# Kernel optimization log

Measured on AMD Instinct MI355X. Metric: run time of the kernel, lower is better.

## Reference

```python
import jax, jax.numpy as jnp
import numpy as np

N_NODES = 100000
N_EDGES = 1600000
D = 128
NEG_SLOPE = 0.01  # torch F.leaky_relu default


def setup_inputs() -> dict:
    key = jax.random.key(0)
    k1, k2, k3, k4, k5 = jax.random.split(key, 5)
    nfeat = jax.random.normal(k1, (N_NODES, D), dtype=jnp.float32)
    edge_src = jax.random.randint(k2, (N_EDGES,), 0, N_NODES, dtype=jnp.int32)
    edge_dst = jax.random.randint(k3, (N_EDGES,), 0, N_NODES, dtype=jnp.int32)
    edge_w = jax.random.uniform(k4, (N_EDGES,), dtype=jnp.float32)
    W = jax.random.normal(k5, (D, D), dtype=jnp.float32) * (1.0 / np.sqrt(D))
    return {"nfeat": nfeat, "edge_src": edge_src, "edge_dst": edge_dst,
            "edge_w": edge_w, "W": W}


def reference(nfeat, edge_src, edge_dst, edge_w, W):
    # message: m_e = h[src_e] * w_e  (u_mul_e)
    msg = nfeat[edge_src] * edge_w[:, None]          # [E, D]
    # reduce: h_neighbor[v] = sum_{e: dst(e)=v} m_e  (fn.sum)
    h_neighbor = jax.ops.segment_sum(msg, edge_dst, num_segments=nfeat.shape[0])  # [N, D]
    # Bi-interaction residual: leaky_relu(Linear(h * h_neighbor)); dropout = identity (eval)
    out = jax.nn.leaky_relu((nfeat * h_neighbor) @ W.T, negative_slope=NEG_SLOPE)
    return out
```

## Files before the change

### kernel.cpp

```cpp
#include <hip/hip_runtime.h>
#include <hip/hip_fp16.h>

#define NNODES 100000
#define NEDGES 1600000
#define DIM    128
#define NEG_SLOPE 0.01f
#define NB_SCAN ((NNODES + 1023) / 1024)
#define NPART 8
#define PART_SZ ((NNODES + NPART - 1) / NPART)
#define GEMM_TILES ((NNODES + 63) / 64)

typedef _Float16     v8h __attribute__((ext_vector_type(8)));
typedef float        v4f __attribute__((ext_vector_type(4)));
typedef int          v4i __attribute__((ext_vector_type(4)));
typedef int          v2i __attribute__((ext_vector_type(2)));
typedef float        v4x __attribute__((ext_vector_type(4)));
typedef unsigned int v2u __attribute__((ext_vector_type(2)));
typedef unsigned int v4u __attribute__((ext_vector_type(4)));

static inline size_t align256(size_t x) { return (x + 255) & ~(size_t)255; }

union HU { unsigned int u; __half2 h; };

__global__ __launch_bounds__(256) void zero_f32(float* __restrict__ p, int n4) {
    int i = blockIdx.x * blockDim.x + threadIdx.x;
    int stride = gridDim.x * blockDim.x;
    float4 z = make_float4(0.f, 0.f, 0.f, 0.f);
    for (; i < n4; i += stride) ((float4*)p)[i] = z;
}

__global__ __launch_bounds__(256) void prep(const float* __restrict__ nf,
                                            __half* __restrict__ nf16,
                                            int* __restrict__ counts) {
    int i = blockIdx.x * 256 + threadIdx.x;
    int stride = gridDim.x * 256;
    for (int j = i; j < NNODES * DIM / 4; j += stride) {
        v4x v = __builtin_nontemporal_load((const v4x*)nf + j);
        HU a, b;
        a.h = __float22half2_rn(make_float2(v.x, v.y));
        b.h = __float22half2_rn(make_float2(v.z, v.w));
        ((uint2*)nf16)[j] = make_uint2(a.u, b.u);
    }
    v4i z = (v4i){0, 0, 0, 0};
    for (int j = i; j < NNODES / 4; j += stride)
        *((v4i*)counts + j) = z;
}

__global__ __launch_bounds__(256) void hist_dst4(const int* __restrict__ edst,
                                                 int* __restrict__ counts) {
    int i = blockIdx.x * 256 + threadIdx.x;
    if (i < NEDGES / 4) {
        v4i d = __builtin_nontemporal_load((const v4i*)edst + i);
        atomicAdd(&counts[d.x], 1);
        atomicAdd(&counts[d.y], 1);
        atomicAdd(&counts[d.z], 1);
        atomicAdd(&counts[d.w], 1);
    }
}

__global__ __launch_bounds__(256) void scan1(const int* __restrict__ counts,
                                             int* __restrict__ offsets,
                                             int* __restrict__ blocksum) {
    __shared__ int lds[256];
    int tid = threadIdx.x;
    int base = blockIdx.x * 1024 + tid * 4;
    int c0 = (base + 0 < NNODES) ? counts[base + 0] : 0;
    int c1 = (base + 1 < NNODES) ? counts[base + 1] : 0;
    int c2 = (base + 2 < NNODES) ? counts[base + 2] : 0;
    int c3 = (base + 3 < NNODES) ? counts[base + 3] : 0;
    int t = c0 + c1 + c2 + c3;
    lds[tid] = t;
    __syncthreads();
    for (int d = 1; d < 256; d <<= 1) {
        int v = lds[tid];
        int add = (tid >= d) ? lds[tid - d] : 0;
        __syncthreads();
        lds[tid] = v + add;
        __syncthreads();
    }
    int incl = lds[tid];
    int excl = incl - t;
    if (base + 0 < NNODES) offsets[base + 0] = excl;
    if (base + 1 < NNODES) offsets[base + 1] = excl + c0;
    if (base + 2 < NNODES) offsets[base + 2] = excl + c0 + c1;
    if (base + 3 < NNODES) offsets[base + 3] = excl + c0 + c1 + c2;
    if (tid == 255) blocksum[blockIdx.x] = incl;
}

__global__ __launch_bounds__(128) void scan2p(int* __restrict__ blocksum, int nb) {
    __shared__ int lds[128];
    int tid = threadIdx.x;
    int v = (tid < nb) ? blocksum[tid] : 0;
    lds[tid] = v;
    __syncthreads();
    for (int d = 1; d < 128; d <<= 1) {
        int x = lds[tid];
        int add = (tid >= d) ? lds[tid - d] : 0;
        __syncthreads();
        lds[tid] = x + add;
        __syncthreads();
    }
    if (tid < nb) blocksum[tid] = lds[tid] - v;
}

__global__ __launch_bounds__(256) void scan3(int* __restrict__ offsets,
                                             const int* __restrict__ blocksum,
                                             int* __restrict__ cursor) {
    int add = blocksum[blockIdx.x];
    int base = blockIdx.x * 1024 + threadIdx.x * 4;
    #pragma unroll
    for (int i = 0; i < 4; ++i) {
        int idx = base + i;
        if (idx < NNODES) { int o = offsets[idx] + add; offsets[idx] = o; cursor[idx] = o; }
    }
}

__global__ __launch_bounds__(256) void fill_part(const int* __restrict__ esrc,
                                                 const int* __restrict__ edst,
                                                 const float* __restrict__ ew,
                                                 int* __restrict__ cursor,
                                                 int2* __restrict__ bins) {
    int part = blockIdx.x & (NPART - 1);
    int lo = part * PART_SZ;
    int hi = lo + PART_SZ;
    int t = (blockIdx.x >> 3) * 256 + threadIdx.x;
    int stride = (gridDim.x >> 3) * 256;
    int nq = NEDGES / 4;
    for (int i = t; i < nq; i += stride) {
        v4i d = __builtin_nontemporal_load((const v4i*)edst + i);
        int e = i * 4;
        if (d.x >= lo && d.x < hi) {
            int s = __builtin_nontemporal_load(esrc + e + 0);
            float w = __builtin_nontemporal_load(ew + e + 0);
            int p = atomicAdd(&cursor[d.x], 1);
            bins[p] = make_int2(s, __float_as_int(w));
        }
        if (d.y >= lo && d.y < hi) {
            int s = __builtin_nontemporal_load(esrc + e + 1);
            float w = __builtin_nontemporal_load(ew + e + 1);
            int p = atomicAdd(&cursor[d.y], 1);
            bins[p] = make_int2(s, __float_as_int(w));
        }
        if (d.z >= lo && d.z < hi) {
            int s = __builtin_nontemporal_load(esrc + e + 2);
            float w = __builtin_nontemporal_load(ew + e + 2);
            int p = atomicAdd(&cursor[d.z], 1);
            bins[p] = make_int2(s, __float_as_int(w));
        }
        if (d.w >= lo && d.w < hi) {
            int s = __builtin_nontemporal_load(esrc + e + 3);
            float w = __builtin_nontemporal_load(ew + e + 3);
            int p = atomicAdd(&cursor[d.w], 1);
            bins[p] = make_int2(s, __float_as_int(w));
        }
    }
}

__global__ __launch_bounds__(256) void pull_x16(const __half* __restrict__ nf16,
                                                const int* __restrict__ offsets,
                                                const int* __restrict__ counts,
                                                const int2* __restrict__ bins,
                                                __half* __restrict__ x16) {
    int gid = blockIdx.x * 256 + threadIdx.x;
    int v = gid >> 5;
    int lane = gid & 31;
    if (v >= NNODES) return;
    int start = offsets[v];
    int end = start + counts[v];
    const uint2* nf2 = (const uint2*)nf16;
    float4 a0 = make_float4(0.f, 0.f, 0.f, 0.f);
    float4 a1 = make_float4(0.f, 0.f, 0.f, 0.f);
    float4 a2 = make_float4(0.f, 0.f, 0.f, 0.f);
    float4 a3 = make_float4(0.f, 0.f, 0.f, 0.f);
    int k = start;
    for (; k + 4 <= end; k += 4) {
        v2i e0 = __builtin_nontemporal_load((const v2i*)bins + k);
        v2i e1 = __builtin_nontemporal_load((const v2i*)bins + k + 1);
        v2i e2 = __builtin_nontemporal_load((const v2i*)bins + k + 2);
        v2i e3 = __builtin_nontemporal_load((const v2i*)bins + k + 3);
        uint2 u0 = nf2[(size_t)e0.x * 32 + lane];
        uint2 u1 = nf2[(size_t)e1.x * 32 + lane];
        uint2 u2 = nf2[(size_t)e2.x * 32 + lane];
        uint2 u3 = nf2[(size_t)e3.x * 32 + lane];
        float w0 = __int_as_float(e0.y), w1 = __int_as_float(e1.y);
        float w2 = __int_as_float(e2.y), w3 = __int_as_float(e3.y);
        HU h; float2 f;
        h.u = u0.x; f = __half22float2(h.h); a0.x += w0 * f.x; a0.y += w0 * f.y;
        h.u = u0.y; f = __half22float2(h.h); a0.z += w0 * f.x; a0.w += w0 * f.y;
        h.u = u1.x; f = __half22float2(h.h); a1.x += w1 * f.x; a1.y += w1 * f.y;
        h.u = u1.y; f = __half22float2(h.h); a1.z += w1 * f.x; a1.w += w1 * f.y;
        h.u = u2.x; f = __half22float2(h.h); a2.x += w2 * f.x; a2.y += w2 * f.y;
        h.u = u2.y; f = __half22float2(h.h); a2.z += w2 * f.x; a2.w += w2 * f.y;
        h.u = u3.x; f = __half22float2(h.h); a3.x += w3 * f.x; a3.y += w3 * f.y;
        h.u = u3.y; f = __half22float2(h.h); a3.z += w3 * f.x; a3.w += w3 * f.y;
    }
    for (; k < end; ++k) {
        v2i e = __builtin_nontemporal_load((const v2i*)bins + k);
        float w = __int_as_float(e.y);
        uint2 u = nf2[(size_t)e.x * 32 + lane];
        HU h; float2 f;
        h.u = u.x; f = __half22float2(h.h); a0.x += w * f.x; a0.y += w * f.y;
        h.u = u.y; f = __half22float2(h.h); a0.z += w * f.x; a0.w += w * f.y;
    }
    float4 acc;
    acc.x = (a0.x + a1.x) + (a2.x + a3.x);
    acc.y = (a0.y + a1.y) + (a2.y + a3.y);
    acc.z = (a0.z + a1.z) + (a2.z + a3.z);
    acc.w = (a0.w + a1.w) + (a2.w + a3.w);
    uint2 un = nf2[(size_t)v * 32 + lane];
    HU h; float2 f;
    h.u = un.x; f = __half22float2(h.h); acc.x *= f.x; acc.y *= f.y;
    h.u = un.y; f = __half22float2(h.h); acc.z *= f.x; acc.w *= f.y;
    HU o0, o1;
    o0.h = __float22half2_rn(make_float2(acc.x, acc.y));
    o1.h = __float22half2_rn(make_float2(acc.z, acc.w));
    v2u ov = (v2u){o0.u, o1.u};
    __builtin_nontemporal_store(ov, (v2u*)x16 + (size_t)v * 32 + lane);
}

__global__ __launch_bounds__(256) void gemm16(const __half* __restrict__ x16,
                                              const float* __restrict__ W,
                                              float* __restrict__ out) {
    __shared__ _Float16 Wl[128 * 128];
    __shared__ _Float16 Xl[64 * 128];
    int tid = threadIdx.x;

    const float4* Wg = (const float4*)W;
    for (int i = tid; i < 2048; i += 256) {
        int r = i >> 4, c = i & 15;
        float4 lo = Wg[(r * 128 + c * 8) >> 2];
        float4 hi = Wg[((r * 128 + c * 8) >> 2) + 1];
        v8h h;
        h[0] = (_Float16)lo.x; h[1] = (_Float16)lo.y; h[2] = (_Float16)lo.z; h[3] = (_Float16)lo.w;
        h[4] = (_Float16)hi.x; h[5] = (_Float16)hi.y; h[6] = (_Float16)hi.z; h[7] = (_Float16)hi.w;
        *(v8h*)&Wl[r * 128 + (c ^ (r & 7)) * 8] = h;
    }

    int rbase = blockIdx.x * 64;
    for (int i = tid; i < 1024; i += 256) {
        int r = i >> 4, c = i & 15;
        int grow = rbase + r;
        v4u u = (v4u){0u, 0u, 0u, 0u};
        if (grow < NNODES)
            u = __builtin_nontemporal_load((const v4u*)x16 + (size_t)grow * 16 + c);
        *(v4u*)&Xl[r * 128 + (c ^ (r & 7)) * 8] = u;
    }
    __syncthreads();

    int wave = tid >> 6;
    int lane = tid & 63;
    int n = lane & 15;
    int g = lane >> 4;

    v4f acc[8];
    #pragma unroll
    for (int jb = 0; jb < 8; ++jb) acc[jb] = (v4f){0.f, 0.f, 0.f, 0.f};

    #pragma unroll
    for (int kb = 0; kb < 4; ++kb) {
        v8h a = *(v8h*)&Xl[(wave * 16 + n) * 128 + (((kb * 4 + g) ^ (n & 7)) * 8)];
        #pragma unroll
        for (int jb = 0; jb < 8; ++jb) {
            v8h b = *(v8h*)&Wl[(jb * 16 + n) * 128 + (((kb * 4 + g) ^ (n & 7)) * 8)];
            acc[jb] = __builtin_amdgcn_mfma_f32_16x16x32_f16(a, b, acc[jb], 0, 0, 0);
        }
    }

    int row0 = rbase + wave * 16 + g * 4;
    #pragma unroll
    for (int jb = 0; jb < 8; ++jb) {
        #pragma unroll
        for (int reg = 0; reg < 4; ++reg) {
            int r = row0 + reg;
            if (r < NNODES) {
                float v = acc[jb][reg];
                v = v >= 0.f ? v : NEG_SLOPE * v;
                __builtin_nontemporal_store(v, out + (size_t)r * 128 + jb * 16 + n);
            }
        }
    }
}

__global__ __launch_bounds__(256) void scatter_edges(
    const float* __restrict__ nfeat, const int* __restrict__ esrc,
    const int* __restrict__ edst, const float* __restrict__ ew,
    float* __restrict__ hn) {
    long long t = (long long)blockIdx.x * 256 + threadIdx.x;
    int e = (int)(t >> 5);
    if (e >= NEDGES) return;
    int lane = (int)(t & 31);
    int s = esrc[e];
    int d = edst[e];
    float w = ew[e];
    float4 v = ((const float4*)(nfeat + (size_t)s * DIM))[lane];
    float* o = hn + (size_t)d * DIM + lane * 4;
    unsafeAtomicAdd(o + 0, v.x * w);
    unsafeAtomicAdd(o + 1, v.y * w);
    unsafeAtomicAdd(o + 2, v.z * w);
    unsafeAtomicAdd(o + 3, v.w * w);
}

__global__ __launch_bounds__(256) void elem_mul(const float* __restrict__ nfeat,
                                                float* __restrict__ hn, int n4) {
    int i = blockIdx.x * blockDim.x + threadIdx.x;
    int stride = gridDim.x * blockDim.x;
    for (; i < n4; i += stride) {
        float4 a = ((const float4*)nfeat)[i];
        float4 b = ((float4*)hn)[i];
        b.x *= a.x; b.y *= a.y; b.z *= a.z; b.w *= a.w;
        ((float4*)hn)[i] = b;
    }
}

__global__ __launch_bounds__(256) void bi_gemm2(
    const float* __restrict__ x, const float* __restrict__ W,
    float* __restrict__ out) {
    extern __shared__ float lds[];
    float4* W4  = (float4*)lds;
    float*  xs  = lds + 128 * 128;
    float4* xs4 = (float4*)xs;
    int tid = threadIdx.x;
    const float4* Wg = (const float4*)W;
    for (int i = tid; i < 128 * 32; i += 256) {
        int j = i >> 5, d4 = i & 31;
        W4[(j << 5) | (d4 ^ ((j >> 2) & 7))] = Wg[i];
    }
    __syncthreads();
    int tx = tid & 31, ty = tid >> 5;
    int j0 = tx << 2, r0 = ty << 2;
    int ntiles = NNODES / 32;
    for (int tile = blockIdx.x; tile < ntiles; tile += gridDim.x) {
        int rbase = tile * 32;
        for (int i = tid; i < 32 * 32; i += 256)
            xs4[i] = ((const float4*)x)[(size_t)rbase * 32 + i];
        __syncthreads();
        float acc[4][4];
        #pragma unroll
        for (int r = 0; r < 4; ++r)
            #pragma unroll
            for (int j = 0; j < 4; ++j) acc[r][j] = 0.f;
        #pragma unroll 4
        for (int d4 = 0; d4 < 32; ++d4) {
            float4 xv[4], wv[4];
            #pragma unroll
            for (int r = 0; r < 4; ++r) xv[r] = xs4[((r0 + r) << 5) | d4];
            #pragma unroll
            for (int j = 0; j < 4; ++j) {
                int jj = j0 + j;
                wv[j] = W4[(jj << 5) | (d4 ^ ((jj >> 2) & 7))];
            }
            #pragma unroll
            for (int r = 0; r < 4; ++r)
                #pragma unroll
                for (int j = 0; j < 4; ++j) {
                    acc[r][j] += xv[r].x * wv[j].x;
                    acc[r][j] += xv[r].y * wv[j].y;
                    acc[r][j] += xv[r].z * wv[j].z;
                    acc[r][j] += xv[r].w * wv[j].w;
                }
        }
        __syncthreads();
        #pragma unroll
        for (int r = 0; r < 4; ++r) {
            float4 o;
            o.x = acc[r][0] >= 0.f ? acc[r][0] : NEG_SLOPE * acc[r][0];
            o.y = acc[r][1] >= 0.f ? acc[r][1] : NEG_SLOPE * acc[r][1];
            o.z = acc[r][2] >= 0.f ? acc[r][2] : NEG_SLOPE * acc[r][2];
            o.w = acc[r][3] >= 0.f ? acc[r][3] : NEG_SLOPE * acc[r][3];
            size_t row = (size_t)(rbase + r0 + r);
            ((float4*)out)[row * (DIM / 4) + tx] = o;
        }
    }
}

extern "C" void kernel_launch(void* const* d_in, const int* in_sizes, int n_in,
                              void* d_out, int out_size, void* d_ws, size_t ws_size,
                              hipStream_t stream) {
    const float* nfeat = (const float*)d_in[0];
    const int*   esrc  = (const int*)d_in[1];
    const int*   edst  = (const int*)d_in[2];
    const float* ew    = (const float*)d_in[3];
    const float* W     = (const float*)d_in[4];
    float* out = (float*)d_out;

    size_t off = 0;
    size_t nf16_off = off;     off += align256((size_t)NNODES * DIM * 2);
    size_t x16_off = off;      off += align256((size_t)NNODES * DIM * 2);
    size_t cnt_off = off;      off += align256((size_t)NNODES * 4);
    size_t ofs_off = off;      off += align256((size_t)NNODES * 4);
    size_t cur_off = off;      off += align256((size_t)NNODES * 4);
    size_t bsum_off = off;     off += align256((size_t)NB_SCAN * 4);
    size_t bins_off = off;     off += align256((size_t)NEDGES * 8);
    size_t need = off;

    char* ws = (char*)d_ws;

    if (ws_size >= need) {
        __half* nf16 = (__half*)(ws + nf16_off);
        __half* x16  = (__half*)(ws + x16_off);
        int* counts = (int*)(ws + cnt_off);
        int* offsets = (int*)(ws + ofs_off);
        int* cursor = (int*)(ws + cur_off);
        int* blocksum = (int*)(ws + bsum_off);
        int2* bins = (int2*)(ws + bins_off);

        prep<<<2048, 256, 0, stream>>>(nfeat, nf16, counts);
        int e4grid = (NEDGES / 4 + 255) / 256;
        hist_dst4<<<e4grid, 256, 0, stream>>>(edst, counts);
        scan1<<<NB_SCAN, 256, 0, stream>>>(counts, offsets, blocksum);
        scan2p<<<1, 128, 0, stream>>>(blocksum, NB_SCAN);
        scan3<<<NB_SCAN, 256, 0, stream>>>(offsets, blocksum, cursor);
        fill_part<<<2048, 256, 0, stream>>>(esrc, edst, ew, cursor, bins);
        int pgrid = (NNODES * 32 + 255) / 256;
        pull_x16<<<pgrid, 256, 0, stream>>>(nf16, offsets, counts, bins, x16);
        gemm16<<<GEMM_TILES, 256, 0, stream>>>(x16, W, out);
    } else {
        float* hn = (float*)ws;
        hipFuncSetAttribute((const void*)bi_gemm2,
                            hipFuncAttributeMaxDynamicSharedMemorySize, 81920);
        zero_f32<<<2048, 256, 0, stream>>>(hn, NNODES * DIM / 4);
        int sgrid = (NEDGES * 32 + 255) / 256;
        scatter_edges<<<sgrid, 256, 0, stream>>>(nfeat, esrc, edst, ew, hn);
        elem_mul<<<2048, 256, 0, stream>>>(nfeat, hn, NNODES * DIM / 4);
        bi_gemm2<<<512, 256, 81920, stream>>>(hn, W, out);
    }
}
```

Before: 277.2 us.

## Pre-split edges into per-partition buckets before histogram and CSR fill

Adds a split pass that buckets each edge (dst, src, weight) into one of eight destination partitions, using block-local counting and one global atomic per partition. The histogram and CSR fill kernels then read only their own partition's compact list instead of every fill block scanning the full edge array and filtering. The aim is to cut redundant edge reads and improve atomic locality on the counts and cursor arrays. The cost is an extra 16-byte-per-edge staging buffer and one more pass over the edges. A fixed per-partition capacity (PCAP) silently drops edges if a partition overflows, which only holds for roughly uniform destination distributions.

New measurement: 337.5 us. 1.22x slower.

```diff
diff --git a/kernel.cpp b/kernel.cpp
--- a/kernel.cpp
+++ b/kernel.cpp
@@ -8,6 +8,7 @@
 #define NB_SCAN ((NNODES + 1023) / 1024)
 #define NPART 8
 #define PART_SZ ((NNODES + NPART - 1) / NPART)
+#define PCAP 220000
 #define GEMM_TILES ((NNODES + 63) / 64)
 
 typedef _Float16     v8h __attribute__((ext_vector_type(8)));
@@ -31,7 +32,8 @@
 
 __global__ __launch_bounds__(256) void prep(const float* __restrict__ nf,
                                             __half* __restrict__ nf16,
-                                            int* __restrict__ counts) {
+                                            int* __restrict__ counts,
+                                            int* __restrict__ pcur) {
     int i = blockIdx.x * 256 + threadIdx.x;
     int stride = gridDim.x * 256;
     for (int j = i; j < NNODES * DIM / 4; j += stride) {
@@ -44,17 +46,45 @@
     v4i z = (v4i){0, 0, 0, 0};
     for (int j = i; j < NNODES / 4; j += stride)
         *((v4i*)counts + j) = z;
-}
-
-__global__ __launch_bounds__(256) void hist_dst4(const int* __restrict__ edst,
+    if (i < NPART) pcur[i] = 0;
+}
+
+__global__ __launch_bounds__(256) void split_edges(const int* __restrict__ esrc,
+                                                   const int* __restrict__ edst,
+                                                   const float* __restrict__ ew,
+                                                   int* __restrict__ pcur,
+                                                   int4* __restrict__ triples) {
+    __shared__ int bcnt[NPART];
+    __shared__ int gbase[NPART];
+    int tid = threadIdx.x;
+    int e = blockIdx.x * 256 + tid;
+    int dst = __builtin_nontemporal_load(edst + e);
+    int src = __builtin_nontemporal_load(esrc + e);
+    float w = __builtin_nontemporal_load(ew + e);
+    int part = dst / PART_SZ;
+    if (tid < NPART) bcnt[tid] = 0;
+    __syncthreads();
+    int lrank = atomicAdd(&bcnt[part], 1);
+    __syncthreads();
+    if (tid < NPART) gbase[tid] = atomicAdd(&pcur[tid], bcnt[tid]);
+    __syncthreads();
+    int slot = gbase[part] + lrank;
+    if (slot < PCAP)
+        triples[(size_t)part * PCAP + slot] = make_int4(dst, src, __float_as_int(w), 0);
+}
+
+__global__ __launch_bounds__(256) void hist_part(const int4* __restrict__ triples,
+                                                 const int* __restrict__ pcur,
                                                  int* __restrict__ counts) {
-    int i = blockIdx.x * 256 + threadIdx.x;
-    if (i < NEDGES / 4) {
-        v4i d = __builtin_nontemporal_load((const v4i*)edst + i);
-        atomicAdd(&counts[d.x], 1);
-        atomicAdd(&counts[d.y], 1);
-        atomicAdd(&counts[d.z], 1);
-        atomicAdd(&counts[d.w], 1);
+    int part = blockIdx.x & (NPART - 1);
+    int n = pcur[part];
+    if (n > PCAP) n = PCAP;
+    const int4* base = triples + (size_t)part * PCAP;
+    int t = (blockIdx.x >> 3) * 256 + threadIdx.x;
+    int stride = (gridDim.x >> 3) * 256;
+    for (int i = t; i < n; i += stride) {
+        v4i tr = __builtin_nontemporal_load((const v4i*)base + i);
+        atomicAdd(&counts[tr.x], 1);
     }
 }
 
@@ -115,44 +145,20 @@
     }
 }
 
-__global__ __launch_bounds__(256) void fill_part(const int* __restrict__ esrc,
-                                                 const int* __restrict__ edst,
-                                                 const float* __restrict__ ew,
-                                                 int* __restrict__ cursor,
-                                                 int2* __restrict__ bins) {
+__global__ __launch_bounds__(256) void fill_part2(const int4* __restrict__ triples,
+                                                  const int* __restrict__ pcur,
+                                                  int* __restrict__ cursor,
+                                                  int2* __restrict__ bins) {
     int part = blockIdx.x & (NPART - 1);
-    int lo = part * PART_SZ;
-    int hi = lo + PART_SZ;
+    int n = pcur[part];
+    if (n > PCAP) n = PCAP;
+    const int4* base = triples + (size_t)part * PCAP;
     int t = (blockIdx.x >> 3) * 256 + threadIdx.x;
     int stride = (gridDim.x >> 3) * 256;
-    int nq = NEDGES / 4;
-    for (int i = t; i < nq; i += stride) {
-        v4i d = __builtin_nontemporal_load((const v4i*)edst + i);
-        int e = i * 4;
-        if (d.x >= lo && d.x < hi) {
-            int s = __builtin_nontemporal_load(esrc + e + 0);
-            float w = __builtin_nontemporal_load(ew + e + 0);
-            int p = atomicAdd(&cursor[d.x], 1);
-            bins[p] = make_int2(s, __float_as_int(w));
-        }
-        if (d.y >= lo && d.y < hi) {
-            int s = __builtin_nontemporal_load(esrc + e + 1);
-            float w = __builtin_nontemporal_load(ew + e + 1);
-            int p = atomicAdd(&cursor[d.y], 1);
-            bins[p] = make_int2(s, __float_as_int(w));
-        }
-        if (d.z >= lo && d.z < hi) {
-            int s = __builtin_nontemporal_load(esrc + e + 2);
-            float w = __builtin_nontemporal_load(ew + e + 2);
-            int p = atomicAdd(&cursor[d.z], 1);
-            bins[p] = make_int2(s, __float_as_int(w));
-        }
-        if (d.w >= lo && d.w < hi) {
-            int s = __builtin_nontemporal_load(esrc + e + 3);
-            float w = __builtin_nontemporal_load(ew + e + 3);
-            int p = atomicAdd(&cursor[d.w], 1);
-            bins[p] = make_int2(s, __float_as_int(w));
-        }
+    for (int i = t; i < n; i += stride) {
+        v4i tr = __builtin_nontemporal_load((const v4i*)base + i);
+        int p = atomicAdd(&cursor[tr.x], 1);
+        bins[p] = make_int2(tr.y, tr.z);
     }
 }
 
@@ -281,6 +287,51 @@
     }
 }
 
+__global__ __launch_bounds__(256) void hist_dst4(const int* __restrict__ edst,
+                                                 int* __restrict__ counts) {
+    int i = blockIdx.x * 256 + threadIdx.x;
+    if (i < NEDGES / 4) {
+        int4 d = ((const int4*)edst)[i];
+        atomicAdd(&counts[d.x], 1);
+        atomicAdd(&counts[d.y], 1);
+        atomicAdd(&counts[d.z], 1);
+        atomicAdd(&counts[d.w], 1);
+    }
+}
+
+__global__ __launch_bounds__(256) void fill_part(const int* __restrict__ esrc,
+                                                 const int* __restrict__ edst,
+                                                 const float* __restrict__ ew,
+                                                 int* __restrict__ cursor,
+                                                 int2* __restrict__ bins) {
+    int part = blockIdx.x & (NPART - 1);
+    int lo = part * PART_SZ;
+    int hi = lo + PART_SZ;
+    int t = (blockIdx.x >> 3) * 256 + threadIdx.x;
+    int stride = (gridDim.x >> 3) * 256;
+    int nq = NEDGES / 4;
+    for (int i = t; i < nq; i += stride) {
+        int4 d = ((const int4*)edst)[i];
+        int e = i * 4;
+        if (d.x >= lo && d.x < hi) {
+            int p = atomicAdd(&cursor[d.x], 1);
+            bins[p] = make_int2(esrc[e + 0], __float_as_int(ew[e + 0]));
+        }
+        if (d.y >= lo && d.y < hi) {
+            int p = atomicAdd(&cursor[d.y], 1);
+            bins[p] = make_int2(esrc[e + 1], __float_as_int(ew[e + 1]));
+        }
+        if (d.z >= lo && d.z < hi) {
+            int p = atomicAdd(&cursor[d.z], 1);
+            bins[p] = make_int2(esrc[e + 2], __float_as_int(ew[e + 2]));
+        }
+        if (d.w >= lo && d.w < hi) {
+            int p = atomicAdd(&cursor[d.w], 1);
+            bins[p] = make_int2(esrc[e + 3], __float_as_int(ew[e + 3]));
+        }
+    }
+}
+
 __global__ __launch_bounds__(256) void scatter_edges(
     const float* __restrict__ nfeat, const int* __restrict__ esrc,
     const int* __restrict__ edst, const float* __restrict__ ew,
@@ -389,28 +440,42 @@
     size_t cnt_off = off;      off += align256((size_t)NNODES * 4);
     size_t ofs_off = off;      off += align256((size_t)NNODES * 4);
     size_t cur_off = off;      off += align256((size_t)NNODES * 4);
+    size_t pcur_off = off;     off += align256((size_t)NPART * 4);
     size_t bsum_off = off;     off += align256((size_t)NB_SCAN * 4);
     size_t bins_off = off;     off += align256((size_t)NEDGES * 8);
-    size_t need = off;
+    size_t need_mid = off;
+    size_t trip_off = off;     off += align256((size_t)NPART * PCAP * 16);
+    size_t need_full = off;
 
     char* ws = (char*)d_ws;
 
-    if (ws_size >= need) {
+    if (ws_size >= need_mid) {
         __half* nf16 = (__half*)(ws + nf16_off);
         __half* x16  = (__half*)(ws + x16_off);
         int* counts = (int*)(ws + cnt_off);
         int* offsets = (int*)(ws + ofs_off);
         int* cursor = (int*)(ws + cur_off);
+        int* pcur = (int*)(ws + pcur_off);
         int* blocksum = (int*)(ws + bsum_off);
         int2* bins = (int2*)(ws + bins_off);
-
-        prep<<<2048, 256, 0, stream>>>(nfeat, nf16, counts);
-        int e4grid = (NEDGES / 4 + 255) / 256;
-        hist_dst4<<<e4grid, 256, 0, stream>>>(edst, counts);
-        scan1<<<NB_SCAN, 256, 0, stream>>>(counts, offsets, blocksum);
-        scan2p<<<1, 128, 0, stream>>>(blocksum, NB_SCAN);
-        scan3<<<NB_SCAN, 256, 0, stream>>>(offsets, blocksum, cursor);
-        fill_part<<<2048, 256, 0, stream>>>(esrc, edst, ew, cursor, bins);
+        int4* triples = (int4*)(ws + trip_off);
+
+        prep<<<2048, 256, 0, stream>>>(nfeat, nf16, counts, pcur);
+        if (ws_size >= need_full) {
+            split_edges<<<NEDGES / 256, 256, 0, stream>>>(esrc, edst, ew, pcur, triples);
+            hist_part<<<2048, 256, 0, stream>>>(triples, pcur, counts);
+            scan1<<<NB_SCAN, 256, 0, stream>>>(counts, offsets, blocksum);
+            scan2p<<<1, 128, 0, stream>>>(blocksum, NB_SCAN);
+            scan3<<<NB_SCAN, 256, 0, stream>>>(offsets, blocksum, cursor);
+            fill_part2<<<2048, 256, 0, stream>>>(triples, pcur, cursor, bins);
+        } else {
+            int e4grid = (NEDGES / 4 + 255) / 256;
+            hist_dst4<<<e4grid, 256, 0, stream>>>(edst, counts);
+            scan1<<<NB_SCAN, 256, 0, stream>>>(counts, offsets, blocksum);
+            scan2p<<<1, 128, 0, stream>>>(blocksum, NB_SCAN);
+            scan3<<<NB_SCAN, 256, 0, stream>>>(offsets, blocksum, cursor);
+            fill_part<<<2048, 256, 0, stream>>>(esrc, edst, ew, cursor, bins);
+        }
         int pgrid = (NNODES * 32 + 255) / 256;
         pull_x16<<<pgrid, 256, 0, stream>>>(nf16, offsets, counts, bins, x16);
         gemm16<<<GEMM_TILES, 256, 0, stream>>>(x16, W, out);
```
